# Kernel tuning notes

Measured on AMD Instinct MI355X. Metric: run time of the kernel, lower is better.

## Reference

```python
import jax, jax.numpy as jnp
import numpy as np

LAYER_SIZE = [784, 128, 64, 10]
ACTIVE_FUN = ["relu", "relu", "linear"]
BATCH = 65536


def setup_inputs() -> dict:
    key = jax.random.key(0)
    k_x, k0, k1, k2 = jax.random.split(key, 4)
    X = jax.random.normal(k_x, (BATCH, LAYER_SIZE[0]), dtype=jnp.float32)
    # weights mimic torch init: 0.1 * rand(in+1, out)
    W0 = 0.1 * jax.random.uniform(k0, (LAYER_SIZE[0] + 1, LAYER_SIZE[1]), dtype=jnp.float32)
    W1 = 0.1 * jax.random.uniform(k1, (LAYER_SIZE[1] + 1, LAYER_SIZE[2]), dtype=jnp.float32)
    W2 = 0.1 * jax.random.uniform(k2, (LAYER_SIZE[2] + 1, LAYER_SIZE[3]), dtype=jnp.float32)
    return {"X": X, "W0": W0, "W1": W1, "W2": W2}


def _act(h, name):
    if name == "sigmoid":
        return jax.nn.sigmoid(h)
    if name == "relu":
        return jnp.maximum(h, 0.0)
    if name == "tanh":
        return jnp.tanh(h)
    return h  # linear


def _mlp(X, weights):
    h = X
    for W, act in zip(weights, ACTIVE_FUN):
        # bias folded in: concat a column of ones (original concats scalar 1 per sample)
        ones = jnp.ones((h.shape[0], 1), dtype=h.dtype)
        h = jnp.concatenate([h, ones], axis=1) @ W
        h = _act(h, act)
    return h


def reference(X, W0, W1, W2):
    # Batched equivalent of the per-sample Python loop: returns [B, 10] predictions
    return _mlp(X, [W0, W1, W2])
```

## Files before the change

### kernel.cpp

```cpp
#include <hip/hip_runtime.h>

typedef unsigned short u16;
typedef __attribute__((ext_vector_type(4))) float f32x4;
typedef __attribute__((ext_vector_type(8))) short short8;

#define D0 784
#define D1 128
#define D2 64
#define D3 10
#define KS0 25
#define KS1 4
#define KS2 2

#define WS_W0P 0
#define WS_W1P 204800
#define WS_W2P 221184
#define WS_B0  223232
#define WS_B1  223744
#define WS_B2  224000

__device__ __forceinline__ u16 f2bf(float f) {
  union { float f; unsigned u; } v; v.f = f;
  unsigned u = v.u;
  return (u16)((u + 0x7fffu + ((u >> 16) & 1u)) >> 16);
}

__device__ __forceinline__ int swz(int c, int kk) {
  return c * 32 + (((kk >> 3) ^ ((c >> 1) & 3)) << 3) + (kk & 7);
}

__global__ void prep_kernel(const float* __restrict__ W0, const float* __restrict__ W1,
                            const float* __restrict__ W2, u16* __restrict__ w0p,
                            u16* __restrict__ w1p, u16* __restrict__ w2p,
                            float* __restrict__ b0, float* __restrict__ b1,
                            float* __restrict__ b2) {
  int idx = blockIdx.x * 256 + threadIdx.x;
  if (idx < 25 * 128 * 32) {
    int ks = idx / 4096, rem = idx % 4096, c = rem >> 5, kk = rem & 31;
    int k = ks * 32 + kk;
    float v = (k < D0) ? W0[k * D1 + c] : 0.f;
    w0p[ks * 4096 + swz(c, kk)] = f2bf(v);
    return;
  }
  idx -= 25 * 128 * 32;
  if (idx < 4 * 64 * 32) {
    int ks = idx / 2048, rem = idx % 2048, c = rem >> 5, kk = rem & 31;
    int k = ks * 32 + kk;
    w1p[ks * 2048 + swz(c, kk)] = f2bf(W1[k * D2 + c]);
    return;
  }
  idx -= 4 * 64 * 32;
  if (idx < 2 * 16 * 32) {
    int ks = idx / 512, rem = idx % 512, c = rem >> 5, kk = rem & 31;
    int k = ks * 32 + kk;
    float v = (c < D3) ? W2[k * D3 + c] : 0.f;
    w2p[ks * 512 + swz(c, kk)] = f2bf(v);
    return;
  }
  idx -= 2 * 16 * 32;
  if (idx < 128) { b0[idx] = W0[D0 * D1 + idx]; return; }
  idx -= 128;
  if (idx < 64) { b1[idx] = W1[D1 * D2 + idx]; return; }
  idx -= 64;
  if (idx < 16) { b2[idx] = (idx < D3) ? W2[D2 * D3 + idx] : 0.f; }
}

__device__ __forceinline__ void gload_lds16(const void* g, void* l) {
  __builtin_amdgcn_global_load_lds((const __attribute__((address_space(1))) void*)g,
                                   (__attribute__((address_space(3))) void*)l, 16, 0, 0);
}

__global__ __launch_bounds__(256) void mlp_fused(
    const float* __restrict__ X, const u16* __restrict__ w0p,
    const u16* __restrict__ w1p, const float* __restrict__ b0,
    const float* __restrict__ b1, const float* __restrict__ b2,
    float* __restrict__ out) {
  __shared__ __attribute__((aligned(16))) u16 smW0[2][4096];
  __shared__ __attribute__((aligned(16))) u16 smW12[9216];
  __shared__ __attribute__((aligned(16))) u16 smH0[4][16][136];
  __shared__ __attribute__((aligned(16))) u16 smH1[4][16][72];

  const int t = threadIdx.x;
  const int lane = t & 63;
  const int wv = t >> 6;
  const int q = lane >> 4;
  const int lr = lane & 15;

  {
    const char* src = (const char*)w1p;
    char* dst = (char*)smW12;
    for (int off = wv * 1024; off < 18432; off += 4096)
      gload_lds16(src + off + lane * 16, dst + off);
  }
  auto stageW0 = [&](int buf, int ks) {
    const char* src = (const char*)(w0p + ks * 4096) + wv * 2048 + lane * 16;
    char* dst = (char*)&smW0[buf][0] + wv * 2048;
    gload_lds16(src, dst);
    gload_lds16(src + 1024, dst + 1024);
  };

  const int row = blockIdx.x * 64 + wv * 16 + lr;
  const float* xrow = X + (size_t)row * D0;

  f32x4 acc0[8];
#pragma unroll
  for (int f = 0; f < 8; ++f) acc0[f] = (f32x4){0.f, 0.f, 0.f, 0.f};

  f32x4 xa, xb;
  {
    const f32x4* xp = (const f32x4*)(xrow + q * 8);
    xa = xp[0]; xb = xp[1];
  }
  stageW0(0, 0);
  __syncthreads();

  int buf = 0;
  for (int ks = 0; ks < KS0; ++ks) {
    if (ks + 1 < KS0) stageW0(buf ^ 1, ks + 1);
    f32x4 na = (f32x4){0.f, 0.f, 0.f, 0.f}, nb = (f32x4){0.f, 0.f, 0.f, 0.f};
    if (ks + 1 < KS0) {
      int kb = (ks + 1) * 32 + q * 8;
      if (kb < D0) {
        const f32x4* xp = (const f32x4*)(xrow + kb);
        na = xp[0]; nb = xp[1];
      }
    }
    short8 a;
    a[0] = (short)f2bf(xa[0]); a[1] = (short)f2bf(xa[1]);
    a[2] = (short)f2bf(xa[2]); a[3] = (short)f2bf(xa[3]);
    a[4] = (short)f2bf(xb[0]); a[5] = (short)f2bf(xb[1]);
    a[6] = (short)f2bf(xb[2]); a[7] = (short)f2bf(xb[3]);
    const u16* smb = &smW0[buf][0];
#pragma unroll
    for (int f = 0; f < 8; ++f) {
      int c = f * 16 + lr;
      int js = q ^ ((c >> 1) & 3);
      short8 b = *(const short8*)(smb + c * 32 + js * 8);
      acc0[f] = __builtin_amdgcn_mfma_f32_16x16x32_bf16(a, b, acc0[f], 0, 0, 0);
    }
    __syncthreads();
    xa = na; xb = nb; buf ^= 1;
  }

#pragma unroll
  for (int f = 0; f < 8; ++f) {
    int c = f * 16 + lr;
    float bb = b0[c];
#pragma unroll
    for (int r = 0; r < 4; ++r) {
      float v = acc0[f][r] + bb;
      smH0[wv][q * 4 + r][c] = f2bf(fmaxf(v, 0.f));
    }
  }

  f32x4 acc1[4];
#pragma unroll
  for (int f = 0; f < 4; ++f) acc1[f] = (f32x4){0.f, 0.f, 0.f, 0.f};
  const u16* h0row = &smH0[wv][lr][0];
#pragma unroll
  for (int ks = 0; ks < KS1; ++ks) {
    short8 a = *(const short8*)(h0row + ks * 32 + q * 8);
#pragma unroll
    for (int f = 0; f < 4; ++f) {
      int c = f * 16 + lr;
      int js = q ^ ((c >> 1) & 3);
      short8 b = *(const short8*)(smW12 + ks * 2048 + c * 32 + js * 8);
      acc1[f] = __builtin_amdgcn_mfma_f32_16x16x32_bf16(a, b, acc1[f], 0, 0, 0);
    }
  }
#pragma unroll
  for (int f = 0; f < 4; ++f) {
    int c = f * 16 + lr;
    float bb = b1[c];
#pragma unroll
    for (int r = 0; r < 4; ++r)
      smH1[wv][q * 4 + r][c] = f2bf(fmaxf(acc1[f][r] + bb, 0.f));
  }

  f32x4 acc2 = (f32x4){0.f, 0.f, 0.f, 0.f};
  const u16* h1row = &smH1[wv][lr][0];
  const u16* w2sm = smW12 + 8192;
#pragma unroll
  for (int ks = 0; ks < KS2; ++ks) {
    short8 a = *(const short8*)(h1row + ks * 32 + q * 8);
    int js = q ^ ((lr >> 1) & 3);
    short8 b = *(const short8*)(w2sm + ks * 512 + lr * 32 + js * 8);
    acc2 = __builtin_amdgcn_mfma_f32_16x16x32_bf16(a, b, acc2, 0, 0, 0);
  }
  if (lr < D3) {
    float bb = b2[lr];
#pragma unroll
    for (int r = 0; r < 4; ++r) {
      int rowg = blockIdx.x * 64 + wv * 16 + q * 4 + r;
      out[rowg * D3 + lr] = acc2[r] + bb;
    }
  }
}

extern "C" void kernel_launch(void* const* d_in, const int* in_sizes, int n_in,
                              void* d_out, int out_size, void* d_ws, size_t ws_size,
                              hipStream_t stream) {
  const float* X  = (const float*)d_in[0];
  const float* W0 = (const float*)d_in[1];
  const float* W1 = (const float*)d_in[2];
  const float* W2 = (const float*)d_in[3];
  float* out = (float*)d_out;
  char* ws = (char*)d_ws;
  u16* w0p = (u16*)(ws + WS_W0P);
  u16* w1p = (u16*)(ws + WS_W1P);
  u16* w2p = (u16*)(ws + WS_W2P);
  float* b0 = (float*)(ws + WS_B0);
  float* b1 = (float*)(ws + WS_B1);
  float* b2 = (float*)(ws + WS_B2);

  prep_kernel<<<437, 256, 0, stream>>>(W0, W1, W2, w0p, w1p, w2p, b0, b1, b2);
  mlp_fused<<<65536 / 64, 256, 0, stream>>>(X, w0p, w1p, b0, b1, b2, out);
}
```

Before: 52.42 us.

## Reuse W0 LDS buffer for hidden activations, swizzle them, and pack bf16 conversions

```diff
diff --git a/kernel.cpp b/kernel.cpp
--- a/kernel.cpp
+++ b/kernel.cpp
@@ -70,15 +70,17 @@
                                    (__attribute__((address_space(3))) void*)l, 16, 0, 0);
 }
 
-__global__ __launch_bounds__(256) void mlp_fused(
+__device__ __forceinline__ void cvtpk(unsigned& d, float lo, float hi) {
+  asm("v_cvt_pk_bf16_f32 %0, %1, %2" : "=v"(d) : "v"(lo), "v"(hi));
+}
+
+__global__ __launch_bounds__(256, 4) void mlp_fused(
     const float* __restrict__ X, const u16* __restrict__ w0p,
     const u16* __restrict__ w1p, const float* __restrict__ b0,
     const float* __restrict__ b1, const float* __restrict__ b2,
     float* __restrict__ out) {
   __shared__ __attribute__((aligned(16))) u16 smW0[2][4096];
   __shared__ __attribute__((aligned(16))) u16 smW12[9216];
-  __shared__ __attribute__((aligned(16))) u16 smH0[4][16][136];
-  __shared__ __attribute__((aligned(16))) u16 smH1[4][16][72];
 
   const int t = threadIdx.x;
   const int lane = t & 63;
@@ -113,6 +115,8 @@
   }
   stageW0(0, 0);
   __syncthreads();
+
+  const int boff = lr * 32 + (q ^ ((lr >> 1) & 3)) * 8;
 
   int buf = 0;
   for (int ks = 0; ks < KS0; ++ks) {
@@ -125,41 +129,44 @@
         na = xp[0]; nb = xp[1];
       }
     }
-    short8 a;
-    a[0] = (short)f2bf(xa[0]); a[1] = (short)f2bf(xa[1]);
-    a[2] = (short)f2bf(xa[2]); a[3] = (short)f2bf(xa[3]);
-    a[4] = (short)f2bf(xb[0]); a[5] = (short)f2bf(xb[1]);
-    a[6] = (short)f2bf(xb[2]); a[7] = (short)f2bf(xb[3]);
+    union { short8 s; unsigned u[4]; } a;
+    cvtpk(a.u[0], xa[0], xa[1]);
+    cvtpk(a.u[1], xa[2], xa[3]);
+    cvtpk(a.u[2], xb[0], xb[1]);
+    cvtpk(a.u[3], xb[2], xb[3]);
     const u16* smb = &smW0[buf][0];
 #pragma unroll
     for (int f = 0; f < 8; ++f) {
-      int c = f * 16 + lr;
-      int js = q ^ ((c >> 1) & 3);
-      short8 b = *(const short8*)(smb + c * 32 + js * 8);
-      acc0[f] = __builtin_amdgcn_mfma_f32_16x16x32_bf16(a, b, acc0[f], 0, 0, 0);
+      short8 b = *(const short8*)(smb + f * 512 + boff);
+      acc0[f] = __builtin_amdgcn_mfma_f32_16x16x32_bf16(a.s, b, acc0[f], 0, 0, 0);
     }
     __syncthreads();
     xa = na; xb = nb; buf ^= 1;
   }
+
+  char* hbase = (char*)&smW0[0][0] + wv * 4096;
 
 #pragma unroll
   for (int f = 0; f < 8; ++f) {
     int c = f * 16 + lr;
     float bb = b0[c];
+    int chb = ((c >> 3) << 4);
+    int cwb = (c & 7) << 1;
 #pragma unroll
     for (int r = 0; r < 4; ++r) {
+      int rr = q * 4 + r;
       float v = acc0[f][r] + bb;
-      smH0[wv][q * 4 + r][c] = f2bf(fmaxf(v, 0.f));
-    }
-  }
+      *(u16*)(hbase + rr * 256 + (chb ^ ((rr & 7) << 4)) + cwb) = f2bf(fmaxf(v, 0.f));
+    }
+  }
+  __builtin_amdgcn_wave_barrier();
 
   f32x4 acc1[4];
 #pragma unroll
   for (int f = 0; f < 4; ++f) acc1[f] = (f32x4){0.f, 0.f, 0.f, 0.f};
-  const u16* h0row = &smH0[wv][lr][0];
 #pragma unroll
   for (int ks = 0; ks < KS1; ++ks) {
-    short8 a = *(const short8*)(h0row + ks * 32 + q * 8);
+    short8 a = *(const short8*)(hbase + lr * 256 + (((ks * 4 + q) ^ (lr & 7)) << 4));
 #pragma unroll
     for (int f = 0; f < 4; ++f) {
       int c = f * 16 + lr;
@@ -172,17 +179,22 @@
   for (int f = 0; f < 4; ++f) {
     int c = f * 16 + lr;
     float bb = b1[c];
-#pragma unroll
-    for (int r = 0; r < 4; ++r)
-      smH1[wv][q * 4 + r][c] = f2bf(fmaxf(acc1[f][r] + bb, 0.f));
-  }
+    int chb = ((c >> 3) << 4);
+    int cwb = (c & 7) << 1;
+#pragma unroll
+    for (int r = 0; r < 4; ++r) {
+      int rr = q * 4 + r;
+      *(u16*)(hbase + rr * 128 + (chb ^ ((rr & 7) << 4)) + cwb) =
+          f2bf(fmaxf(acc1[f][r] + bb, 0.f));
+    }
+  }
+  __builtin_amdgcn_wave_barrier();
 
   f32x4 acc2 = (f32x4){0.f, 0.f, 0.f, 0.f};
-  const u16* h1row = &smH1[wv][lr][0];
   const u16* w2sm = smW12 + 8192;
 #pragma unroll
   for (int ks = 0; ks < KS2; ++ks) {
-    short8 a = *(const short8*)(h1row + ks * 32 + q * 8);
+    short8 a = *(const short8*)(hbase + lr * 128 + (((ks * 4 + q) ^ (lr & 7)) << 4));
     int js = q ^ ((lr >> 1) & 3);
     short8 b = *(const short8*)(w2sm + ks * 512 + lr * 32 + js * 8);
     acc2 = __builtin_amdgcn_mfma_f32_16x16x32_bf16(a, b, acc2, 0, 0, 0);
```

Measured after the change: 45.22 us. -13.7%, faster.
